# Kernel tuning notes

Measured on AMD Instinct MI355X. Metric: run time of the kernel, lower is better.

## Reference

```python
import jax, jax.numpy as jnp
import numpy as np


def setup_inputs() -> dict:
    key = jax.random.key(0)
    k1, k2 = jax.random.split(key)
    N, D = 8192, 1024
    anchor = jax.random.normal(k1, (N, D), dtype=jnp.float32)
    negative = jax.random.normal(k2, (N, D), dtype=jnp.float32)
    return {"anchor": anchor, "negative": negative}


def reference(anchor, negative):
    # MSE(a, n) = mean((a - n)^2) over D = (||a||^2 + ||n||^2 - 2 a.n) / D
    D = anchor.shape[-1]
    a2 = jnp.sum(anchor * anchor, axis=-1, keepdims=True)      # [N, 1]
    n2 = jnp.sum(negative * negative, axis=-1)                  # [N]
    dots = jnp.einsum('id,jd->ij', anchor, negative)            # [N, N]
    mse = (a2 + n2[None, :] - 2.0 * dots) / D                   # [N, N]
    idx = jnp.argmax(mse, axis=1)                               # hardest negative per anchor
    return negative[idx]
```

## Files before the change

### kernel.cpp

```cpp
#include <hip/hip_runtime.h>
#include <hip/hip_bf16.h>
#include <stdint.h>

#define NROWS 8192
#define DIM   1024

typedef __attribute__((ext_vector_type(4))) int    i32x4;
typedef __attribute__((ext_vector_type(4))) float  f32x4;

__device__ __forceinline__ unsigned int f32_key(float val) {
    unsigned int b = __float_as_uint(val);
    b ^= (unsigned int)(((int)b >> 31) | 0x80000000);
    return b;
}
__device__ __forceinline__ float key_val(unsigned long long k) {
    unsigned int b = (unsigned int)(k >> 32);
    b = (b & 0x80000000u) ? (b ^ 0x80000000u) : ~b;
    return __uint_as_float(b);
}
__device__ __forceinline__ void load_lds16(const void* g, void* l) {
    __builtin_amdgcn_global_load_lds((const __attribute__((address_space(1))) void*)g,
                                     (__attribute__((address_space(3))) void*)l, 16, 0, 0);
}

__global__ __launch_bounds__(256) void prep_i8_kernel(const float* __restrict__ A,
                                                      const float* __restrict__ B,
                                                      signed char* __restrict__ Aq,
                                                      signed char* __restrict__ Bq,
                                                      float* __restrict__ fA,
                                                      float* __restrict__ fB,
                                                      float* __restrict__ a2,
                                                      float* __restrict__ n2) {
    const float* src = blockIdx.y ? B : A;
    signed char* qdst = blockIdx.y ? Bq : Aq;
    float* fdst = blockIdx.y ? fB : fA;
    float* sdst = blockIdx.y ? n2 : a2;
    int row  = blockIdx.x * 4 + (threadIdx.x >> 6);
    int lane = threadIdx.x & 63;
    const float* p = src + (size_t)row * DIM;

    float4 v[4];
    double s = 0.0;
    float mx = 0.0f;
#pragma unroll
    for (int q = 0; q < 4; ++q) {
        v[q] = *reinterpret_cast<const float4*>(p + (size_t)(lane + 64 * q) * 4);
        s += (double)v[q].x * v[q].x + (double)v[q].y * v[q].y +
             (double)v[q].z * v[q].z + (double)v[q].w * v[q].w;
        mx = fmaxf(mx, fmaxf(fmaxf(fabsf(v[q].x), fabsf(v[q].y)),
                             fmaxf(fabsf(v[q].z), fabsf(v[q].w))));
    }
#pragma unroll
    for (int m = 32; m >= 1; m >>= 1) {
        s  += __shfl_xor(s, m, 64);
        mx  = fmaxf(mx, __shfl_xor(mx, m, 64));
    }
    mx = fmaxf(mx, 1e-30f);
    const float scale = 127.0f / mx;
#pragma unroll
    for (int q = 0; q < 4; ++q) {
        int q0 = (int)rintf(v[q].x * scale);
        int q1 = (int)rintf(v[q].y * scale);
        int q2 = (int)rintf(v[q].z * scale);
        int q3 = (int)rintf(v[q].w * scale);
        int packed = (q0 & 0xFF) | ((q1 & 0xFF) << 8) | ((q2 & 0xFF) << 16) | (q3 << 24);
        *reinterpret_cast<int*>(qdst + (size_t)row * DIM + (size_t)(lane + 64 * q) * 4) = packed;
    }
    if (lane == 0) { sdst[row] = (float)s; fdst[row] = mx / 127.0f; }
}

__global__ __launch_bounds__(256, 3) void mfma_i8_kernel(
        const signed char* __restrict__ Aq,
        const signed char* __restrict__ Bq,
        const float* __restrict__ fA, const float* __restrict__ fB,
        const float* __restrict__ a2, const float* __restrict__ n2,
        unsigned long long* __restrict__ cand ) {
    __shared__ signed char lds[2][128 * 128];

    const int tid  = threadIdx.x;
    const int w    = tid >> 6;
    const int lane = tid & 63;
    const int row0 = blockIdx.x * 128;
    const int col0 = blockIdx.y * 128;
    const int wr = w >> 1, wc = w & 1;
    const int g = lane >> 4, m = lane & 15;

    i32x4 acc[4][4];
#pragma unroll
    for (int r = 0; r < 4; ++r)
#pragma unroll
        for (int c = 0; c < 4; ++c) acc[r][c] = (i32x4)0;

    const signed char* gA = Aq + (size_t)row0 * DIM;
    const signed char* gB = Bq + (size_t)col0 * DIM;

    for (int kt = 0; kt < DIM; kt += 128) {
#pragma unroll
        for (int p = 0; p < 4; ++p) {
            int li  = p * 256 + tid;
            int row = li >> 3;
            int ck  = li & 7;
            int cg  = ck ^ (row & 7);
            load_lds16(gA + (size_t)row * DIM + kt + cg * 16,
                       (char*)&lds[0][0] + (size_t)li * 16);
            load_lds16(gB + (size_t)row * DIM + kt + cg * 16,
                       (char*)&lds[1][0] + (size_t)li * 16);
        }
        __syncthreads();
#pragma unroll
        for (int ks = 0; ks < 2; ++ks) {
            i32x4 af[4], bf[4];
#pragma unroll
            for (int r = 0; r < 4; ++r) {
                int arow = wr * 64 + r * 16 + m;
                int ch   = (ks * 4 + g) ^ (arow & 7);
                af[r] = *(const i32x4*)((const char*)&lds[0][0] + arow * 128 + ch * 16);
                int brow = wc * 64 + r * 16 + m;
                int ch2  = (ks * 4 + g) ^ (brow & 7);
                bf[r] = *(const i32x4*)((const char*)&lds[1][0] + brow * 128 + ch2 * 16);
            }
#pragma unroll
            for (int r = 0; r < 4; ++r)
#pragma unroll
                for (int c = 0; c < 4; ++c)
                    acc[r][c] = __builtin_amdgcn_mfma_i32_16x16x64_i8(af[r], bf[c], acc[r][c], 0, 0, 0);
        }
        __syncthreads();
    }

    const int colbase = col0 + wc * 64;
    const int cb = blockIdx.y * 2 + wc;
    float n2v[4], fbv[4];
#pragma unroll
    for (int c = 0; c < 4; ++c) {
        n2v[c] = n2[colbase + c * 16 + m];
        fbv[c] = fB[colbase + c * 16 + m];
    }
#pragma unroll
    for (int r = 0; r < 4; ++r) {
#pragma unroll
        for (int j = 0; j < 4; ++j) {
            int row = row0 + wr * 64 + r * 16 + g * 4 + j;
            float arow = a2[row];
            float far  = fA[row];
            unsigned long long k1 = 0ull, k2 = 0ull;
#pragma unroll
            for (int c = 0; c < 4; ++c) {
                int col = colbase + c * 16 + m;
                float dot = (float)acc[r][c][j] * far * fbv[c];
                float t = arow + n2v[c];
                t = t - 2.0f * dot;
                float val = t * (1.0f / 1024.0f);
                unsigned long long key =
                    ((unsigned long long)f32_key(val) << 32) |
                    (unsigned long long)(0xFFFFFFFFu - (unsigned)col);
                if (key > k1) { k2 = k1; k1 = key; } else if (key > k2) { k2 = key; }
            }
#pragma unroll
            for (int s = 1; s < 16; s <<= 1) {
                unsigned long long o1 = __shfl_xor(k1, s, 64);
                unsigned long long o2 = __shfl_xor(k2, s, 64);
                unsigned long long hi = k1 > o1 ? k1 : o1;
                unsigned long long md = k1 > o1 ? o1 : k1;
                unsigned long long l2 = k2 > o2 ? k2 : o2;
                k1 = hi; k2 = md > l2 ? md : l2;
            }
            if (m == 0) {
                unsigned long long* p = &cand[((size_t)row * 128 + cb) * 2];
                p[0] = k1; p[1] = k2;
            }
        }
    }
}

#define DELTA 1.5e-2f
__global__ __launch_bounds__(256) void refine_gather_kernel(
        const float* __restrict__ A, const float* __restrict__ B,
        const float* __restrict__ a2, const float* __restrict__ n2,
        const unsigned long long* __restrict__ cand,
        float* __restrict__ out) {
    int row  = blockIdx.x * 4 + (threadIdx.x >> 6);
    int lane = threadIdx.x & 63;
    const unsigned long long* cp = cand + (size_t)row * 256;

    unsigned long long k[4];
#pragma unroll
    for (int q = 0; q < 4; ++q) k[q] = cp[lane + 64 * q];

    unsigned long long mx = k[0];
#pragma unroll
    for (int q = 1; q < 4; ++q) if (k[q] > mx) mx = k[q];
#pragma unroll
    for (int s = 1; s < 64; s <<= 1) {
        unsigned long long o = __shfl_xor(mx, s, 64);
        if (o > mx) mx = o;
    }
    const float thr = key_val(mx) - DELTA;

    const float* ap = A + (size_t)row * DIM;
    const double a2row = (double)a2[row];
    double bestv = -1.0e300;
    int    bestc = 0x7FFFFFFF;

#pragma unroll
    for (int q = 0; q < 4; ++q) {
        float kv = key_val(k[q]);
        int   kc = (int)(0xFFFFFFFFu - (unsigned int)(k[q] & 0xFFFFFFFFull));
        unsigned long long mask = __ballot(kv >= thr);
        while (mask) {
            int src = __ffsll((long long)mask) - 1;
            mask &= mask - 1;
            int col = __shfl(kc, src, 64);
            const float* bp = B + (size_t)col * DIM;
            double part = 0.0;
#pragma unroll
            for (int u = 0; u < 4; ++u) {
                float4 va = reinterpret_cast<const float4*>(ap)[lane + 64 * u];
                float4 vb = reinterpret_cast<const float4*>(bp)[lane + 64 * u];
                part += (double)va.x * vb.x + (double)va.y * vb.y +
                        (double)va.z * vb.z + (double)va.w * vb.w;
            }
#pragma unroll
            for (int s = 1; s < 64; s <<= 1) part += __shfl_xor(part, s, 64);
            double val = (a2row + (double)n2[col] - 2.0 * part) * (1.0 / 1024.0);
            if (val > bestv || (val == bestv && col < bestc)) { bestv = val; bestc = col; }
        }
    }

    const float4* srcp = reinterpret_cast<const float4*>(B + (size_t)bestc * DIM);
    float4*       dstp = reinterpret_cast<float4*>(out + (size_t)row * DIM);
#pragma unroll
    for (int u = 0; u < 4; ++u) dstp[lane + 64 * u] = srcp[lane + 64 * u];
}

__global__ __launch_bounds__(256) void sumsq_kernel(const float* __restrict__ A,
                                                    const float* __restrict__ B,
                                                    float* __restrict__ a2,
                                                    float* __restrict__ n2) {
    const float* src = (blockIdx.y == 0) ? A : B;
    float*       dst = (blockIdx.y == 0) ? a2 : n2;
    int row  = blockIdx.x * 4 + (threadIdx.x >> 6);
    int lane = threadIdx.x & 63;
    const float* p = src + (size_t)row * DIM;
    double s = 0.0;
#pragma unroll
    for (int q = 0; q < 4; ++q) {
        float4 v = *reinterpret_cast<const float4*>(p + (size_t)(lane + 64 * q) * 4);
        s += (double)v.x * v.x + (double)v.y * v.y + (double)v.z * v.z + (double)v.w * v.w;
    }
#pragma unroll
    for (int m = 32; m >= 1; m >>= 1) s += __shfl_xor(s, m, 64);
    if (lane == 0) dst[row] = (float)s;
}

__global__ __launch_bounds__(256) void mse_argmax_kernel(
        const float* __restrict__ A, const float* __restrict__ B,
        const float* __restrict__ a2, const float* __restrict__ n2,
        unsigned long long* __restrict__ best) {
    __shared__ float As[16][132];
    __shared__ float Bs[16][132];
    const int tid = threadIdx.x;
    const int tx = tid & 15, ty = tid >> 4;
    const int row0 = blockIdx.x * 128;
    const int col0 = blockIdx.y * 128;
    float acc[8][8];
#pragma unroll
    for (int r = 0; r < 8; ++r)
#pragma unroll
        for (int c = 0; c < 8; ++c) acc[r][c] = 0.0f;
    for (int kt = 0; kt < DIM; kt += 16) {
#pragma unroll
        for (int p = 0; p < 2; ++p) {
            int li = p * 256 + tid;
            int r  = li >> 2;
            int s4 = li & 3;
            float4 va = *reinterpret_cast<const float4*>(&A[(size_t)(row0 + r) * DIM + kt + s4 * 4]);
            float4 vb = *reinterpret_cast<const float4*>(&B[(size_t)(col0 + r) * DIM + kt + s4 * 4]);
            As[s4 * 4 + 0][r] = va.x; As[s4 * 4 + 1][r] = va.y;
            As[s4 * 4 + 2][r] = va.z; As[s4 * 4 + 3][r] = va.w;
            Bs[s4 * 4 + 0][r] = vb.x; Bs[s4 * 4 + 1][r] = vb.y;
            Bs[s4 * 4 + 2][r] = vb.z; Bs[s4 * 4 + 3][r] = vb.w;
        }
        __syncthreads();
#pragma unroll
        for (int kk = 0; kk < 16; ++kk) {
            float af[8], bfv[8];
#pragma unroll
            for (int r = 0; r < 8; ++r) af[r] = As[kk][ty + 16 * r];
#pragma unroll
            for (int c = 0; c < 8; ++c) bfv[c] = Bs[kk][tx + 16 * c];
#pragma unroll
            for (int r = 0; r < 8; ++r)
#pragma unroll
                for (int c = 0; c < 8; ++c) acc[r][c] = fmaf(af[r], bfv[c], acc[r][c]);
        }
        __syncthreads();
    }
#pragma unroll
    for (int r = 0; r < 8; ++r) {
        const int row = row0 + ty + 16 * r;
        const float arow = a2[row];
        unsigned long long bestk = 0ull;
#pragma unroll
        for (int c = 0; c < 8; ++c) {
            const int col = col0 + tx + 16 * c;
            float t = arow + n2[col];
            t = t - 2.0f * acc[r][c];
            const float val = t * (1.0f / 1024.0f);
            unsigned long long key =
                ((unsigned long long)f32_key(val) << 32) |
                (unsigned long long)(0xFFFFFFFFu - (unsigned)col);
            if (key > bestk) bestk = key;
        }
#pragma unroll
        for (int mm = 1; mm < 16; mm <<= 1) {
            unsigned long long other = __shfl_xor(bestk, mm, 16);
            if (other > bestk) bestk = other;
        }
        if (tx == 0) atomicMax(&best[row], bestk);
    }
}

__global__ __launch_bounds__(256) void gather_kernel(
        const float* __restrict__ B,
        const unsigned long long* __restrict__ best,
        float* __restrict__ out) {
    const int row = blockIdx.x;
    const unsigned int col = 0xFFFFFFFFu - (unsigned int)(best[row] & 0xFFFFFFFFull);
    const float4* src = reinterpret_cast<const float4*>(B + (size_t)col * DIM);
    float4*       dst = reinterpret_cast<float4*>(out + (size_t)row * DIM);
    dst[threadIdx.x] = src[threadIdx.x];
}

extern "C" void kernel_launch(void* const* d_in, const int* in_sizes, int n_in,
                              void* d_out, int out_size, void* d_ws, size_t ws_size,
                              hipStream_t stream) {
    const float* anchor   = (const float*)d_in[0];
    const float* negative = (const float*)d_in[1];
    float* out = (float*)d_out;
    char* ws = (char*)d_ws;

    const size_t qplane    = (size_t)NROWS * DIM;
    const size_t candBytes = (size_t)NROWS * 256 * sizeof(unsigned long long);
    const size_t SC        = 32768;
    const size_t need_i8   = 2 * qplane + 4 * SC + candBytes;

    if (ws_size >= need_i8) {
        signed char* Aq = (signed char*)(ws);
        signed char* Bq = (signed char*)(ws + qplane);
        float* fA = (float*)(ws + 2 * qplane);
        float* fB = (float*)(ws + 2 * qplane + SC);
        float* a2 = (float*)(ws + 2 * qplane + 2 * SC);
        float* n2 = (float*)(ws + 2 * qplane + 3 * SC);
        unsigned long long* cand = (unsigned long long*)(ws + 2 * qplane + 4 * SC);

        prep_i8_kernel<<<dim3(NROWS / 4, 2), 256, 0, stream>>>(
            anchor, negative, Aq, Bq, fA, fB, a2, n2);
        mfma_i8_kernel<<<dim3(NROWS / 128, NROWS / 128), 256, 0, stream>>>(
            Aq, Bq, fA, fB, a2, n2, cand);
        refine_gather_kernel<<<NROWS / 4, 256, 0, stream>>>(
            anchor, negative, a2, n2, cand, out);
    } else {
        float* a2 = (float*)(ws);
        float* n2 = (float*)(ws + 32768);
        unsigned long long* best = (unsigned long long*)(ws + 65536);
        hipMemsetAsync(best, 0, NROWS * sizeof(unsigned long long), stream);
        sumsq_kernel<<<dim3(NROWS / 4, 2), 256, 0, stream>>>(anchor, negative, a2, n2);
        mse_argmax_kernel<<<dim3(NROWS / 128, NROWS / 128), 256, 0, stream>>>(anchor, negative, a2, n2, best);
        gather_kernel<<<NROWS, 256, 0, stream>>>(negative, best, out);
    }
}
```

Before: 166.6 us.

## Double-buffer LDS tiles with async global-to-LDS prefetch in int8 GEMM

Splits LDS into two buffers and prefetches K-tiles two steps ahead using direct global-to-LDS loads, waiting with explicit vmcnt counts and raw barriers instead of __syncthreads. The goal is to overlap global memory latency with MFMA compute. It doubles LDS use to 64KB and lowers the occupancy hint from 3 to 2 blocks per CU. The vmcnt(8) count assumes exactly 8 outstanding loads per stage, which is fragile if the compiler reorders memory operations.

```diff
diff --git a/kernel.cpp b/kernel.cpp
--- a/kernel.cpp
+++ b/kernel.cpp
@@ -69,13 +69,13 @@
     if (lane == 0) { sdst[row] = (float)s; fdst[row] = mx / 127.0f; }
 }
 
-__global__ __launch_bounds__(256, 3) void mfma_i8_kernel(
+__global__ __launch_bounds__(256, 2) void mfma_i8_kernel(
         const signed char* __restrict__ Aq,
         const signed char* __restrict__ Bq,
         const float* __restrict__ fA, const float* __restrict__ fB,
         const float* __restrict__ a2, const float* __restrict__ n2,
         unsigned long long* __restrict__ cand ) {
-    __shared__ signed char lds[2][128 * 128];
+    __shared__ signed char lds[2][2][128 * 128];
 
     const int tid  = threadIdx.x;
     const int w    = tid >> 6;
@@ -94,19 +94,32 @@
     const signed char* gA = Aq + (size_t)row0 * DIM;
     const signed char* gB = Bq + (size_t)col0 * DIM;
 
-    for (int kt = 0; kt < DIM; kt += 128) {
+    auto stage = [&](int t, int buf) {
 #pragma unroll
         for (int p = 0; p < 4; ++p) {
             int li  = p * 256 + tid;
             int row = li >> 3;
             int ck  = li & 7;
             int cg  = ck ^ (row & 7);
-            load_lds16(gA + (size_t)row * DIM + kt + cg * 16,
-                       (char*)&lds[0][0] + (size_t)li * 16);
-            load_lds16(gB + (size_t)row * DIM + kt + cg * 16,
-                       (char*)&lds[1][0] + (size_t)li * 16);
-        }
-        __syncthreads();
+            load_lds16(gA + (size_t)row * DIM + t * 128 + cg * 16,
+                       (char*)&lds[buf][0][0] + (size_t)li * 16);
+            load_lds16(gB + (size_t)row * DIM + t * 128 + cg * 16,
+                       (char*)&lds[buf][1][0] + (size_t)li * 16);
+        }
+    };
+
+    stage(0, 0);
+    stage(1, 1);
+
+#pragma unroll
+    for (int t = 0; t < 8; ++t) {
+        if (t < 7) { asm volatile("s_waitcnt vmcnt(8)" ::: "memory"); }
+        else       { asm volatile("s_waitcnt vmcnt(0)" ::: "memory"); }
+        __builtin_amdgcn_s_barrier();
+        __builtin_amdgcn_sched_barrier(0);
+
+        const signed char* la = &lds[t & 1][0][0];
+        const signed char* lb = &lds[t & 1][1][0];
 #pragma unroll
         for (int ks = 0; ks < 2; ++ks) {
             i32x4 af[4], bf[4];
@@ -114,10 +127,10 @@
             for (int r = 0; r < 4; ++r) {
                 int arow = wr * 64 + r * 16 + m;
                 int ch   = (ks * 4 + g) ^ (arow & 7);
-                af[r] = *(const i32x4*)((const char*)&lds[0][0] + arow * 128 + ch * 16);
+                af[r] = *(const i32x4*)((const char*)la + arow * 128 + ch * 16);
                 int brow = wc * 64 + r * 16 + m;
                 int ch2  = (ks * 4 + g) ^ (brow & 7);
-                bf[r] = *(const i32x4*)((const char*)&lds[1][0] + brow * 128 + ch2 * 16);
+                bf[r] = *(const i32x4*)((const char*)lb + brow * 128 + ch2 * 16);
             }
 #pragma unroll
             for (int r = 0; r < 4; ++r)
@@ -125,7 +138,10 @@
                 for (int c = 0; c < 4; ++c)
                     acc[r][c] = __builtin_amdgcn_mfma_i32_16x16x64_i8(af[r], bf[c], acc[r][c], 0, 0, 0);
         }
-        __syncthreads();
+
+        __builtin_amdgcn_sched_barrier(0);
+        __builtin_amdgcn_s_barrier();
+        if (t < 6) stage(t + 2, t & 1);
     }
 
     const int colbase = col0 + wc * 64;
```

Result: slower. 182.7 us (+9.6%).
